# Performance work log

Hardware: AMD Instinct MI355X
Metric: run time of the kernel (lower is better)

The kernel has to match this reference:

```python
import jax, jax.numpy as jnp
import numpy as np

D = 1024        # embed_dim
NH = 16         # num_heads
DH = D // NH    # head_dim
FFN = 2048      # ffn_hidden_dim
E = 8           # num_experts
K = 2           # top_k
B, T = 2, 1024


def setup_inputs() -> dict:
    key = jax.random.key(0)
    ks = jax.random.split(key, 6)
    s = 0.02
    return {
        "x": jax.random.normal(ks[0], (B, T, D), jnp.float32),
        "ln1_g": jnp.ones((D,), jnp.float32),
        "ln1_b": jnp.zeros((D,), jnp.float32),
        "qkv_w": jax.random.normal(ks[1], (D, 3 * D), jnp.float32) * s,   # [in,out]
        "out_w": jax.random.normal(ks[2], (D, D), jnp.float32) * s,
        "ln2_g": jnp.ones((D,), jnp.float32),
        "ln2_b": jnp.zeros((D,), jnp.float32),
        "gate_w": jax.random.normal(ks[3], (D, E), jnp.float32) * s,
        "expert_biases": jnp.zeros((E,), jnp.float32),
        "w1": jax.random.normal(ks[4], (E, D, 2 * FFN), jnp.float32) * s,  # Expert.linear1 stacked
        "w2": jax.random.normal(ks[5], (E, FFN, D), jnp.float32) * s,      # Expert.linear2 stacked
    }


def _layernorm(x, g, b, eps=1e-5):
    mu = x.mean(-1, keepdims=True)
    var = ((x - mu) ** 2).mean(-1, keepdims=True)
    return (x - mu) * jax.lax.rsqrt(var + eps) * g + b


def _rope(x, theta=10000.0):
    # x: [B, T, H, Dh]; torchtune-style interleaved (even, odd) pair rotation, input_pos=None -> 0..T-1
    Tt, Dh = x.shape[1], x.shape[3]
    inv = 1.0 / (theta ** (jnp.arange(0, Dh, 2, dtype=jnp.float32) / Dh))   # [Dh/2]
    ang = jnp.arange(Tt, dtype=jnp.float32)[:, None] * inv[None, :]         # [T, Dh/2]
    cos = jnp.cos(ang)[None, :, None, :]
    sin = jnp.sin(ang)[None, :, None, :]
    x1, x2 = x[..., 0::2], x[..., 1::2]
    return jnp.stack([x1 * cos - x2 * sin, x2 * cos + x1 * sin], axis=-1).reshape(x.shape)


def reference(x, ln1_g, ln1_b, qkv_w, out_w, ln2_g, ln2_b, gate_w, expert_biases, w1, w2):
    Bx, Tx, Dx = x.shape
    # --- attention sub-block ---
    xn = _layernorm(x, ln1_g, ln1_b)
    qkv = (xn @ qkv_w).reshape(Bx, Tx, 3, NH, DH)
    q, k, v = qkv[:, :, 0], qkv[:, :, 1], qkv[:, :, 2]
    q, k = _rope(q), _rope(k)
    q = q.transpose(0, 2, 1, 3)  # [B,H,T,Dh]
    k = k.transpose(0, 2, 1, 3)
    v = v.transpose(0, 2, 1, 3)
    scores = jnp.einsum('bhqd,bhkd->bhqk', q, k) / jnp.sqrt(jnp.float32(DH))
    attn = jax.nn.softmax(scores, axis=-1)   # non-causal (SDPA default)
    o = jnp.einsum('bhqk,bhkd->bhqd', attn, v).transpose(0, 2, 1, 3).reshape(Bx, Tx, Dx)
    x = x + o @ out_w

    # --- MoE sub-block ---
    xn2 = _layernorm(x, ln2_g, ln2_b)
    gate_scores = xn2 @ gate_w + expert_biases             # [B,T,E]
    topk_vals, topk_idx = jax.lax.top_k(gate_scores, K)    # [B,T,K]
    gates = jax.nn.softmax(topk_vals, axis=-1)             # [B,T,K]
    oh = jax.nn.one_hot(topk_idx, E, dtype=x.dtype)        # [B,T,K,E]
    comb = (oh * gates[..., None]).sum(2)                  # [B,T,E] combine weights
    # dense per-expert SwiGLU FFN (equivalent to masked dispatch: unrouted weight = 0)
    h = jnp.einsum('btd,edh->beth', xn2, w1)               # [B,E,T,2*FFN]
    h1, h2 = jnp.split(h, 2, axis=-1)
    act = jax.nn.silu(h1) * h2
    eo = jnp.einsum('beth,ehd->betd', act, w2)             # [B,E,T,D]
    ffn_out = jnp.einsum('bte,betd->btd', comb, eo)
    x = x + ffn_out

    # --- load-balancing loss ---
    usage = oh.sum((0, 1, 2))                              # [E] token counts
    usage_ratio = usage / usage.sum()
    probs = jax.nn.softmax(gate_scores, axis=-1).mean((0, 1))
    prob_ratio = probs / probs.sum()
    lb_loss = (usage_ratio * prob_ratio).sum() * E
    return x, lb_loss
```

## Files before the change

kernel.cpp:

```cpp
#include <hip/hip_runtime.h>
#include <hip/hip_fp16.h>


typedef _Float16 half8 __attribute__((ext_vector_type(8)));
typedef float f32x4 __attribute__((ext_vector_type(4)));

#define DI __device__ __forceinline__

struct Desc { int e, base, rows; };

DI float blockReduceSum(float v, float* red) {
#pragma unroll
    for (int m = 32; m; m >>= 1) v += __shfl_xor(v, m);
    int w = threadIdx.x >> 6;
    if ((threadIdx.x & 63) == 0) red[w] = v;
    __syncthreads();
    v = red[0] + red[1] + red[2] + red[3];
    __syncthreads();
    return v;
}

DI void split2(float v, __half& hi, __half& lo) {
    hi = __float2half(v);
    lo = __float2half((v - __half2float(hi)) * 2048.0f);
}

enum { EPI_RESID = 0, EPI_QKV = 1 };

template<int WM, int WN, int FM, int FN, int EPI>
__global__ __launch_bounds__(256, 2)
void k_gemm_pk(const __half* __restrict__ Ah, const __half* __restrict__ Al, int lda,
               const __half* __restrict__ Bh, const __half* __restrict__ Bl, int ldb,
               float* __restrict__ Cf, int ldc, int M, int N, int K,
               const float* __restrict__ resid,
               __half* __restrict__ qh_p, __half* __restrict__ ql_p,
               __half* __restrict__ kh_p, __half* __restrict__ kl_p,
               __half* __restrict__ vth_p, __half* __restrict__ vtl_p,
               const float* __restrict__ rc, const float* __restrict__ rs)
{
    constexpr int BM = WM * FM * 16, BN = WN * FN * 16;
    constexpr int PITCH = 40;
    __shared__ __half AsH[BM * PITCH], AsL[BM * PITCH];
    __shared__ __half BsH[BN * PITCH], BsL[BN * PITCH];
    const int tid = threadIdx.x;
    const int lane = tid & 63, w = tid >> 6;
    const int l15 = lane & 15, g = lane >> 4;
    const int wm = w / WN, wn = w % WN;
    const int m0 = blockIdx.x * BM, n0 = blockIdx.y * BN;

    f32x4 acc0[FM][FN] = {}; f32x4 acc1[FM][FN] = {};

    for (int k0 = 0; k0 < K; k0 += 32) {
        __syncthreads();
#pragma unroll
        for (int it = 0; it < BM / 64; ++it) {
            int c = it * 256 + tid, row = c >> 2, kg = c & 3;
            long src = (long)(m0 + row) * lda + k0 + kg * 8;
            *(uint4*)&AsH[row * PITCH + kg * 8] = *(const uint4*)(Ah + src);
            *(uint4*)&AsL[row * PITCH + kg * 8] = *(const uint4*)(Al + src);
        }
#pragma unroll
        for (int it = 0; it < BN / 64; ++it) {
            int c = it * 256 + tid, row = c >> 2, kg = c & 3;
            long src = (long)(n0 + row) * ldb + k0 + kg * 8;
            *(uint4*)&BsH[row * PITCH + kg * 8] = *(const uint4*)(Bh + src);
            *(uint4*)&BsL[row * PITCH + kg * 8] = *(const uint4*)(Bl + src);
        }
        __syncthreads();
        half8 ah[FM], al[FM];
#pragma unroll
        for (int i = 0; i < FM; ++i) {
            int ar = (wm * FM * 16 + i * 16 + l15) * PITCH + g * 8;
            ah[i] = *(const half8*)&AsH[ar];
            al[i] = *(const half8*)&AsL[ar];
        }
#pragma unroll
        for (int n = 0; n < FN; ++n) {
            int br = (wn * FN * 16 + n * 16 + l15) * PITCH + g * 8;
            half8 bh = *(const half8*)&BsH[br];
            half8 bl = *(const half8*)&BsL[br];
#pragma unroll
            for (int i = 0; i < FM; ++i) {
                acc0[i][n] = __builtin_amdgcn_mfma_f32_16x16x32_f16(ah[i], bh, acc0[i][n], 0, 0, 0);
                acc1[i][n] = __builtin_amdgcn_mfma_f32_16x16x32_f16(ah[i], bl, acc1[i][n], 0, 0, 0);
                acc1[i][n] = __builtin_amdgcn_mfma_f32_16x16x32_f16(al[i], bh, acc1[i][n], 0, 0, 0);
            }
        }
    }

#pragma unroll
    for (int i = 0; i < FM; ++i)
#pragma unroll
    for (int n = 0; n < FN; ++n)
#pragma unroll
    for (int j = 0; j < 4; ++j) {
        float v = acc0[i][n][j] + acc1[i][n][j] * (1.0f / 2048.0f);
        int gm = m0 + wm * FM * 16 + i * 16 + g * 4 + j;
        int gn = n0 + wn * FN * 16 + n * 16 + l15;
        if constexpr (EPI == EPI_RESID) {
            Cf[(long)gm * ldc + gn] = v + resid[(long)gm * ldc + gn];
        } else {
            int t = gm & 1023, b = gm >> 10;
            float vp = __shfl_xor(v, 1);
            if (gn < 2048) {
                int col = gn & 1023;
                int i2 = (col & 63) >> 1;
                float cv = rc[t * 32 + i2], sv = rs[t * 32 + i2];
                float rot = cv * v + sv * ((lane & 1) ? vp : -vp);
                __half hi_, lo_; split2(rot, hi_, lo_);
                long o = ((long)(b * 16 + (col >> 6)) * 1024 + t) * 64 + (col & 63);
                if (gn < 1024) { qh_p[o] = hi_; ql_p[o] = lo_; }
                else           { kh_p[o] = hi_; kl_p[o] = lo_; }
            } else {
                int col = gn - 2048;
                __half hi_, lo_; split2(v, hi_, lo_);
                long o = ((long)(b * 16 + (col >> 6)) * 64 + (col & 63)) * 1024 + t;
                vth_p[o] = hi_; vtl_p[o] = lo_;
            }
        }
    }
}

__global__ __launch_bounds__(256, 2)
void k_flash(const __half* __restrict__ qh_g, const __half* __restrict__ ql_g,
             const __half* __restrict__ kh_g, const __half* __restrict__ kl_g,
             const __half* __restrict__ vth_g, const __half* __restrict__ vtl_g,
             __half* __restrict__ oh_g, __half* __restrict__ ol_g)
{
    constexpr int P = 72;
    __shared__ __half KsH[64 * P], KsL[64 * P], VsH[64 * P], VsL[64 * P], PsH[64 * P], PsL[64 * P];
    const int tid = threadIdx.x, lane = tid & 63, w = tid >> 6;
    const int l15 = lane & 15, g = lane >> 4;
    const int q0 = blockIdx.x * 64;
    const int bh = blockIdx.y;
    const long base = (long)bh * 65536;

    half8 qhi[2], qlo[2];
    {
        long qoff = base + (long)(q0 + w * 16 + l15) * 64 + g * 8;
        qhi[0] = *(const half8*)(qh_g + qoff); qhi[1] = *(const half8*)(qh_g + qoff + 32);
        qlo[0] = *(const half8*)(ql_g + qoff); qlo[1] = *(const half8*)(ql_g + qoff + 32);
    }

    float m_[4] = {-1e30f, -1e30f, -1e30f, -1e30f};
    float l_[4] = {0.f, 0.f, 0.f, 0.f};
    f32x4 o0[4] = {}, o1[4] = {};

    for (int kt = 0; kt < 16; ++kt) {
        __syncthreads();
#pragma unroll
        for (int it = 0; it < 2; ++it) {
            int c = it * 256 + tid, row = c >> 3, kg = c & 7;
            long src = base + (long)(kt * 64 + row) * 64 + kg * 8;
            *(uint4*)&KsH[row * P + kg * 8] = *(const uint4*)(kh_g + src);
            *(uint4*)&KsL[row * P + kg * 8] = *(const uint4*)(kl_g + src);
            long vs = base + (long)row * 1024 + kt * 64 + kg * 8;
            *(uint4*)&VsH[row * P + kg * 8] = *(const uint4*)(vth_g + vs);
            *(uint4*)&VsL[row * P + kg * 8] = *(const uint4*)(vtl_g + vs);
        }
        __syncthreads();

        f32x4 s0[4] = {}, s1[4] = {};
#pragma unroll
        for (int cf = 0; cf < 4; ++cf) {
            int kr = (cf * 16 + l15) * P + g * 8;
            half8 kh0 = *(const half8*)&KsH[kr], kh1 = *(const half8*)&KsH[kr + 32];
            half8 kl0 = *(const half8*)&KsL[kr], kl1 = *(const half8*)&KsL[kr + 32];
            s0[cf] = __builtin_amdgcn_mfma_f32_16x16x32_f16(qhi[0], kh0, s0[cf], 0, 0, 0);
            s1[cf] = __builtin_amdgcn_mfma_f32_16x16x32_f16(qhi[0], kl0, s1[cf], 0, 0, 0);
            s1[cf] = __builtin_amdgcn_mfma_f32_16x16x32_f16(qlo[0], kh0, s1[cf], 0, 0, 0);
            s0[cf] = __builtin_amdgcn_mfma_f32_16x16x32_f16(qhi[1], kh1, s0[cf], 0, 0, 0);
            s1[cf] = __builtin_amdgcn_mfma_f32_16x16x32_f16(qhi[1], kl1, s1[cf], 0, 0, 0);
            s1[cf] = __builtin_amdgcn_mfma_f32_16x16x32_f16(qlo[1], kh1, s1[cf], 0, 0, 0);
        }

#pragma unroll
        for (int j = 0; j < 4; ++j) {
            float sv[4];
#pragma unroll
            for (int cf = 0; cf < 4; ++cf)
                sv[cf] = (s0[cf][j] + s1[cf][j] * (1.0f / 2048.0f)) * 0.125f;
            float mx = fmaxf(fmaxf(sv[0], sv[1]), fmaxf(sv[2], sv[3]));
#pragma unroll
            for (int msk = 8; msk; msk >>= 1) mx = fmaxf(mx, __shfl_xor(mx, msk));
            float mn = fmaxf(m_[j], mx);
            float r = expf(m_[j] - mn);
            m_[j] = mn;
            float rs = 0.f;
#pragma unroll
            for (int cf = 0; cf < 4; ++cf) {
                float p = expf(sv[cf] - mn);
                rs += p;
                __half hi_, lo_; split2(p, hi_, lo_);
                PsH[(w * 16 + g * 4 + j) * P + cf * 16 + l15] = hi_;
                PsL[(w * 16 + g * 4 + j) * P + cf * 16 + l15] = lo_;
            }
#pragma unroll
            for (int msk = 8; msk; msk >>= 1) rs += __shfl_xor(rs, msk);
            l_[j] = l_[j] * r + rs;
#pragma unroll
            for (int df = 0; df < 4; ++df) { o0[df][j] *= r; o1[df][j] *= r; }
        }
        __syncthreads();

        int pr = (w * 16 + l15) * P + g * 8;
        half8 ph0 = *(const half8*)&PsH[pr], ph1 = *(const half8*)&PsH[pr + 32];
        half8 pl0 = *(const half8*)&PsL[pr], pl1 = *(const half8*)&PsL[pr + 32];
#pragma unroll
        for (int df = 0; df < 4; ++df) {
            int vr = (df * 16 + l15) * P + g * 8;
            half8 vh0 = *(const half8*)&VsH[vr], vh1 = *(const half8*)&VsH[vr + 32];
            half8 vl0 = *(const half8*)&VsL[vr], vl1 = *(const half8*)&VsL[vr + 32];
            o0[df] = __builtin_amdgcn_mfma_f32_16x16x32_f16(ph0, vh0, o0[df], 0, 0, 0);
            o1[df] = __builtin_amdgcn_mfma_f32_16x16x32_f16(ph0, vl0, o1[df], 0, 0, 0);
            o1[df] = __builtin_amdgcn_mfma_f32_16x16x32_f16(pl0, vh0, o1[df], 0, 0, 0);
            o0[df] = __builtin_amdgcn_mfma_f32_16x16x32_f16(ph1, vh1, o0[df], 0, 0, 0);
            o1[df] = __builtin_amdgcn_mfma_f32_16x16x32_f16(ph1, vl1, o1[df], 0, 0, 0);
            o1[df] = __builtin_amdgcn_mfma_f32_16x16x32_f16(pl1, vh1, o1[df], 0, 0, 0);
        }
    }

    float invl[4];
#pragma unroll
    for (int j = 0; j < 4; ++j) invl[j] = 1.0f / l_[j];
    const int b = bh >> 4, hh = bh & 15;
#pragma unroll
    for (int df = 0; df < 4; ++df)
#pragma unroll
    for (int j = 0; j < 4; ++j) {
        float v = (o0[df][j] + o1[df][j] * (1.0f / 2048.0f)) * invl[j];
        long orow = (long)b * 1024 + q0 + w * 16 + g * 4 + j;
        int col = hh * 64 + df * 16 + l15;
        __half hi_, lo_; split2(v, hi_, lo_);
        oh_g[orow * 1024 + col] = hi_;
        ol_g[orow * 1024 + col] = lo_;
    }
}

__global__ __launch_bounds__(256) void k_wconv(const float* __restrict__ src,
                                               __half* __restrict__ dst, int R, int C)
{
    src += (long)blockIdx.z * R * C;
    dst += (long)blockIdx.z * R * C;
    __shared__ float t[64][65];
    const int tid = threadIdx.x;
    const int c0 = blockIdx.x * 64, r0 = blockIdx.y * 64;
#pragma unroll
    for (int it = 0; it < 4; ++it) {
        int idx = it * 256 + tid;
        int r = idx >> 4, c4 = (idx & 15) * 4;
        float4 v = *(const float4*)(src + (long)(r0 + r) * C + c0 + c4);
        t[r][c4] = v.x; t[r][c4 + 1] = v.y; t[r][c4 + 2] = v.z; t[r][c4 + 3] = v.w;
    }
    __syncthreads();
#pragma unroll
    for (int it = 0; it < 2; ++it) {
        int idx = it * 256 + tid;
        int orow = idx >> 3, oc = (idx & 7) * 8;
        __half v[8];
#pragma unroll
        for (int j = 0; j < 8; ++j) v[j] = __float2half(t[oc + j][orow]);
        *(uint4*)(dst + (long)(c0 + orow) * R + r0 + oc) = *(uint4*)v;
    }
}

template<bool GATHER, int MODE, int FM, int FN, int WN>
__global__ __launch_bounds__(256, 4)
void k_gemm_moe(const __half* __restrict__ A, int lda, const int* __restrict__ rowidx,
                const Desc* __restrict__ desc, const int* __restrict__ ntiles,
                const __half* __restrict__ Bbase, long sB, int ldb,
                void* __restrict__ Cv, int K, const __half* __restrict__ zp)
{
    if ((int)blockIdx.x >= *ntiles) return;
    Desc d = desc[blockIdx.x];
    const __half* Bp = Bbase + (long)d.e * sB;
    constexpr int WM = 4 / WN;
    constexpr int BM = WM * FM * 16, BN = WN * FN * 16;
    constexpr int ACH = BM / 16, BCH = BN / 16;
    constexpr int NCH = ACH + BCH;
    constexpr int CPW = NCH / 4;
    constexpr int HALF_PER_BUF = NCH * 512;
    __shared__ __half S[2][HALF_PER_BUF];
    const int tid = threadIdx.x, lane = tid & 63, w = tid >> 6;
    const int l15 = lane & 15, g = lane >> 4;
    const int wm = w / WN, wn = w % WN;
    const int n0 = blockIdx.y * (MODE == 0 ? BN / 2 : BN);

    const int dlt = lane >> 2;
    const int kgs = ((lane & 3) ^ ((lane >> 3) & 3)) * 8;
    const __half* src[CPW];
    int loff[CPW];
#pragma unroll
    for (int ci = 0; ci < CPW; ++ci) {
        int chunk = w * CPW + ci;
        loff[ci] = chunk * 512;
        if (chunk < ACH) {
            int row = chunk * 16 + dlt;
            if constexpr (GATHER) {
                bool valid = row < d.rows;
                int ar = valid ? rowidx[d.base + row] : 0;
                src[ci] = valid ? (A + (long)ar * lda + kgs) : (zp + kgs);
            } else {
                src[ci] = A + (long)(d.base + row) * lda + kgs;
            }
        } else {
            int row = (chunk - ACH) * 16 + dlt;
            int srcrow;
            if constexpr (MODE == 0) {
                int pb = row >> 4, w4 = row & 15;
                srcrow = ((pb & 1) ? 2048 : 0) + n0 + (pb >> 1) * 16 + w4;
            } else {
                srcrow = n0 + row;
            }
            src[ci] = Bp + (long)srcrow * ldb + kgs;
        }
    }

    const int sg = (g ^ ((l15 >> 1) & 3)) * 8;
    const int arow = (wm * FM * 16 + l15) * 32 + sg;
    const int brow = BM * 32 + (wn * FN * 16 + l15) * 32 + sg;

#pragma unroll
    for (int ci = 0; ci < CPW; ++ci)
        __builtin_amdgcn_global_load_lds((const void*)(src[ci]),
                                         (void*)&S[0][loff[ci]], 16, 0, 0);
    __syncthreads();

    f32x4 acc[FM][FN] = {};
    int cur = 0;
    for (int k0 = 0; k0 < K; k0 += 32) {
        if (k0 + 32 < K) {
            const __half* sb = &S[cur ^ 1][0];
#pragma unroll
            for (int ci = 0; ci < CPW; ++ci)
                __builtin_amdgcn_global_load_lds((const void*)(src[ci] + k0 + 32),
                                                 (void*)(sb + loff[ci]), 16, 0, 0);
        }
        const __half* sc = &S[cur][0];
        half8 a[FM];
#pragma unroll
        for (int i = 0; i < FM; ++i)
            a[i] = *(const half8*)(sc + arow + i * 512);
#pragma unroll
        for (int n = 0; n < FN; ++n) {
            half8 b = *(const half8*)(sc + brow + n * 512);
#pragma unroll
            for (int i = 0; i < FM; ++i)
                acc[i][n] = __builtin_amdgcn_mfma_f32_16x16x32_f16(a[i], b, acc[i][n], 0, 0, 0);
        }
        __syncthreads();
        cur ^= 1;
    }

    if constexpr (MODE == 0) {
#pragma unroll
        for (int i = 0; i < FM; ++i)
#pragma unroll
        for (int p = 0; p < FN / 2; ++p)
#pragma unroll
        for (int j = 0; j < 4; ++j) {
            int rl = wm * FM * 16 + i * 16 + g * 4 + j;
            float h1 = acc[i][2 * p][j], h2 = acc[i][2 * p + 1][j];
            float a = h1 / (1.0f + expf(-h1)) * h2;
            if (rl >= d.rows) a = 0.0f;
            int jc = n0 + wn * (FN * 8) + p * 16 + l15;
            ((__half*)Cv)[(long)(d.base + rl) * 2048 + jc] = __float2half(a);
        }
    } else {
#pragma unroll
        for (int i = 0; i < FM; ++i)
#pragma unroll
        for (int n = 0; n < FN; ++n)
#pragma unroll
        for (int j = 0; j < 4; ++j) {
            int rl = wm * FM * 16 + i * 16 + g * 4 + j;
            int gn = n0 + wn * FN * 16 + n * 16 + l15;
            ((float*)Cv)[(long)(d.base + rl) * 1024 + gn] = acc[i][n][j];
        }
    }
}

__global__ __launch_bounds__(256) void k_transpose_pk(const float* __restrict__ src,
    __half* __restrict__ dsth, __half* __restrict__ dstl, int R, int C)
{
    __shared__ float t[64][65];
    const int tid = threadIdx.x;
    const int c0 = blockIdx.x * 64, r0 = blockIdx.y * 64;
#pragma unroll
    for (int it = 0; it < 4; ++it) {
        int idx = it * 256 + tid;
        int r = idx >> 4, c4 = (idx & 15) * 4;
        float4 v = *(const float4*)(src + (long)(r0 + r) * C + c0 + c4);
        t[r][c4] = v.x; t[r][c4 + 1] = v.y; t[r][c4 + 2] = v.z; t[r][c4 + 3] = v.w;
    }
    __syncthreads();
#pragma unroll
    for (int it = 0; it < 4; ++it) {
        int idx = it * 256 + tid;
        int orow = idx >> 4, oc = (idx & 15) * 4;
        __half hs[4], ls[4];
#pragma unroll
        for (int m = 0; m < 4; ++m) split2(t[oc + m][orow], hs[m], ls[m]);
        long o = (long)(c0 + orow) * R + r0 + oc;
        *(uint2*)&dsth[o] = *(uint2*)hs;
        *(uint2*)&dstl[o] = *(uint2*)ls;
    }
}

template<int MODE>
__global__ __launch_bounds__(256) void k_ln(const float* __restrict__ X,
    const float* __restrict__ g, const float* __restrict__ bta,
    void* __restrict__ o1, void* __restrict__ o2)
{
    __shared__ float red[4];
    const long row = blockIdx.x;
    const float* xr = X + row * 1024;
    const int c = threadIdx.x * 4;
    float4 v = *(const float4*)(xr + c);
    float mu = blockReduceSum(v.x + v.y + v.z + v.w, red) * (1.0f / 1024.0f);
    float d0 = v.x - mu, d1 = v.y - mu, d2 = v.z - mu, d3 = v.w - mu;
    float var = blockReduceSum(d0 * d0 + d1 * d1 + d2 * d2 + d3 * d3, red) * (1.0f / 1024.0f);
    float rs = 1.0f / sqrtf(var + 1e-5f);
    float4 gv = *(const float4*)(g + c);
    float4 bv = *(const float4*)(bta + c);
    float y[4] = {d0 * rs * gv.x + bv.x, d1 * rs * gv.y + bv.y,
                  d2 * rs * gv.z + bv.z, d3 * rs * gv.w + bv.w};
    if constexpr (MODE == 0) {
        __half hs[4], ls[4];
#pragma unroll
        for (int m = 0; m < 4; ++m) split2(y[m], hs[m], ls[m]);
        *(uint2*)((__half*)o1 + row * 1024 + c) = *(uint2*)hs;
        *(uint2*)((__half*)o2 + row * 1024 + c) = *(uint2*)ls;
    } else {
        *(float4*)((float*)o1 + row * 1024 + c) = make_float4(y[0], y[1], y[2], y[3]);
        __half hs[4];
#pragma unroll
        for (int m = 0; m < 4; ++m) hs[m] = __float2half(y[m]);
        *(uint2*)((__half*)o2 + row * 1024 + c) = *(uint2*)hs;
    }
}

__global__ __launch_bounds__(256) void k_rope_table(float* __restrict__ ct, float* __restrict__ st)
{
    int idx = blockIdx.x * 256 + threadIdx.x;
    int t = idx >> 5, i = idx & 31;
    float inv = 1.0f / (float)pow(10000.0, (double)i / 32.0);
    float ang = (float)t * inv;
    ct[idx] = cosf(ang);
    st[idx] = sinf(ang);
}

__global__ __launch_bounds__(256) void k_gate(const float* __restrict__ xn2,
    const float* __restrict__ gw, const float* __restrict__ eb,
    int* __restrict__ topidx, float* __restrict__ gates,
    float* __restrict__ pprob)
{
    __shared__ float pp[4][8];
    const int lane = threadIdx.x & 63, w = threadIdx.x >> 6;
    const int t = blockIdx.x * 4 + w;
    const float* xr = xn2 + (long)t * 1024;
    float sc[8] = {0, 0, 0, 0, 0, 0, 0, 0};
#pragma unroll
    for (int i = 0; i < 4; ++i) {
        int d = i * 256 + lane * 4;
        float4 xv = *(const float4*)(xr + d);
        float xa[4] = {xv.x, xv.y, xv.z, xv.w};
#pragma unroll
        for (int j = 0; j < 4; ++j) {
            float xx = xa[j];
            const float4* gp = (const float4*)(gw + (long)(d + j) * 8);
            float4 g0 = gp[0], g1 = gp[1];
            sc[0] += xx * g0.x; sc[1] += xx * g0.y; sc[2] += xx * g0.z; sc[3] += xx * g0.w;
            sc[4] += xx * g1.x; sc[5] += xx * g1.y; sc[6] += xx * g1.z; sc[7] += xx * g1.w;
        }
    }
#pragma unroll
    for (int e = 0; e < 8; ++e) {
#pragma unroll
        for (int m = 32; m; m >>= 1) sc[e] += __shfl_xor(sc[e], m);
        sc[e] += eb[e];
    }
    if (lane == 0) {
        int i1 = 0; float v1 = sc[0];
        for (int e = 1; e < 8; ++e) if (sc[e] > v1) { v1 = sc[e]; i1 = e; }
        int i2 = (i1 == 0) ? 1 : 0; float v2 = sc[i2];
        for (int e = 0; e < 8; ++e) if (e != i1 && sc[e] > v2) { v2 = sc[e]; i2 = e; }
        float e2 = expf(v2 - v1);
        gates[t * 2] = 1.0f / (1.0f + e2);
        gates[t * 2 + 1] = e2 / (1.0f + e2);
        topidx[t * 2] = i1; topidx[t * 2 + 1] = i2;
        float mxx = sc[0];
        for (int e = 1; e < 8; ++e) mxx = fmaxf(mxx, sc[e]);
        float se = 0.0f, pe[8];
        for (int e = 0; e < 8; ++e) { pe[e] = expf(sc[e] - mxx); se += pe[e]; }
        float inv = 1.0f / se;
        for (int e = 0; e < 8; ++e) pp[w][e] = pe[e] * inv;
    }
    __syncthreads();
    if (threadIdx.x < 8)
        pprob[(long)blockIdx.x * 8 + threadIdx.x] =
            pp[0][threadIdx.x] + pp[1][threadIdx.x] + pp[2][threadIdx.x] + pp[3][threadIdx.x];
}

__global__ __launch_bounds__(256) void k_route(const int* __restrict__ topidx,
    int* __restrict__ rowidx, int* __restrict__ invpos,
    int* __restrict__ ntiles, Desc* __restrict__ desc, int* __restrict__ cnt)
{
    __shared__ int cnt_s[8], base_s[8], fill[8];
    const int tid = threadIdx.x;
    if (tid < 8) { cnt_s[tid] = 0; fill[tid] = 0; }
    __syncthreads();
    for (int i = tid; i < 4096; i += 256)
        atomicAdd(&cnt_s[topidx[i]], 1);
    __syncthreads();
    if (tid == 0) {
        int tl[8]; int running = 0, maxT = 0;
        for (int e = 0; e < 8; ++e) {
            int ce = cnt_s[e];
            cnt[e] = ce;
            base_s[e] = running;
            tl[e] = (ce + 127) >> 7;
            running += tl[e] * 128;
            if (tl[e] > maxT) maxT = tl[e];
        }
        int nt = 0;
        for (int r = 0; r < maxT; ++r)
            for (int e = 0; e < 8; ++e)
                if (r < tl[e]) {
                    desc[nt].e = e;
                    desc[nt].base = base_s[e] + r * 128;
                    desc[nt].rows = min(128, cnt_s[e] - r * 128);
                    ++nt;
                }
        *ntiles = nt;
    }
    __syncthreads();
    for (int t = tid; t < 2048; t += 256) {
#pragma unroll
        for (int s = 0; s < 2; ++s) {
            int e = topidx[t * 2 + s];
            int p = base_s[e] + atomicAdd(&fill[e], 1);
            rowidx[p] = t;
            invpos[t * 2 + s] = p;
        }
    }
}

__global__ __launch_bounds__(256) void k_combine(const float* __restrict__ x1,
    const float* __restrict__ eo, const int* __restrict__ invpos,
    const float* __restrict__ gates, float* __restrict__ out)
{
    const int t = blockIdx.x, c = threadIdx.x * 4;
    float g0 = gates[t * 2], g1 = gates[t * 2 + 1];
    int p0 = invpos[t * 2], p1 = invpos[t * 2 + 1];
    float4 xv = *(const float4*)(x1 + (long)t * 1024 + c);
    float4 e0 = *(const float4*)(eo + (long)p0 * 1024 + c);
    float4 e1 = *(const float4*)(eo + (long)p1 * 1024 + c);
    float4 o;
    o.x = xv.x + g0 * e0.x + g1 * e1.x;
    o.y = xv.y + g0 * e0.y + g1 * e1.y;
    o.z = xv.z + g0 * e0.z + g1 * e1.z;
    o.w = xv.w + g0 * e0.w + g1 * e1.w;
    *(float4*)(out + (long)t * 1024 + c) = o;
}

__global__ __launch_bounds__(256) void k_loss(const int* __restrict__ cnt,
    const float* __restrict__ pprob, float* __restrict__ out)
{
    __shared__ float m[32][8];
    const int tid = threadIdx.x;
    const int e = tid & 7, g = tid >> 3;
    float local = 0.0f;
    for (int b = g; b < 512; b += 32) local += pprob[b * 8 + e];
    m[g][e] = local;
    __syncthreads();
    if (tid == 0) {
        float us = 0, ps = 0, pe[8], ue[8];
        for (int ee = 0; ee < 8; ++ee) {
            float s = 0;
            for (int gg = 0; gg < 32; ++gg) s += m[gg][ee];
            pe[ee] = s; ps += s;
            ue[ee] = (float)cnt[ee]; us += ue[ee];
        }
        float lb = 0;
        for (int ee = 0; ee < 8; ++ee) lb += (ue[ee] / us) * (pe[ee] / ps);
        out[2097152] = lb * 8.0f;
    }
}

extern "C" void kernel_launch(void* const* d_in, const int* in_sizes, int n_in,
                              void* d_out, int out_size, void* d_ws, size_t ws_size,
                              hipStream_t stream)
{
    const float* x    = (const float*)d_in[0];
    const float* ln1g = (const float*)d_in[1];
    const float* ln1b = (const float*)d_in[2];
    const float* qkvw = (const float*)d_in[3];
    const float* outw = (const float*)d_in[4];
    const float* ln2g = (const float*)d_in[5];
    const float* ln2b = (const float*)d_in[6];
    const float* gw   = (const float*)d_in[7];
    const float* eb   = (const float*)d_in[8];
    const float* w1   = (const float*)d_in[9];
    const float* w2   = (const float*)d_in[10];
    float* out = (float*)d_out;
    char* ws = (char*)d_ws;

    constexpr size_t OFF_QWTH = 0;
    constexpr size_t OFF_QWTL = 6291456;
    constexpr size_t OFF_OWTH = 12582912;
    constexpr size_t OFF_OWTL = 14680064;
    constexpr size_t OFF_XN1H = 16777216;
    constexpr size_t OFF_XN1L = 20971520;
    constexpr size_t OFF_QH   = 25165824;
    constexpr size_t OFF_QL   = 29360128;
    constexpr size_t OFF_KH   = 33554432;
    constexpr size_t OFF_KL   = 37748736;
    constexpr size_t OFF_VTH  = 41943040;
    constexpr size_t OFF_VTL  = 46137344;
    constexpr size_t OFF_OH   = 50331648;
    constexpr size_t OFF_OL   = 54525952;
    constexpr size_t OFF_X1   = 58720256;
    constexpr size_t OFF_XN2F = 67108864;
    constexpr size_t OFF_XN2H = 75497472;
    constexpr size_t OFF_RC   = 79691776;
    constexpr size_t OFF_RS   = 79822848;
    constexpr size_t OFF_IDX  = 79953920;
    constexpr size_t OFF_GATES= 79970304;
    constexpr size_t OFF_INVP = 79986688;
    constexpr size_t OFF_ROWI = 80003072;
    constexpr size_t OFF_CNT  = 80023552;
    constexpr size_t OFF_NT   = 80023616;
    constexpr size_t OFF_DESC = 80023680;
    constexpr size_t OFF_PPROB= 80024704;
    constexpr size_t OFF_ACT  = 80041984;
    constexpr size_t OFF_EO   = 101013504;
    constexpr size_t OFF_W1T  = 121985024;
    constexpr size_t OFF_W2T  = 189093888;

    __half* qwth = (__half*)(ws + OFF_QWTH);
    __half* qwtl = (__half*)(ws + OFF_QWTL);
    __half* owth = (__half*)(ws + OFF_OWTH);
    __half* owtl = (__half*)(ws + OFF_OWTL);
    __half* xn1h = (__half*)(ws + OFF_XN1H);
    __half* xn1l = (__half*)(ws + OFF_XN1L);
    __half* qh   = (__half*)(ws + OFF_QH);
    __half* ql   = (__half*)(ws + OFF_QL);
    __half* kh   = (__half*)(ws + OFF_KH);
    __half* kl   = (__half*)(ws + OFF_KL);
    __half* vth  = (__half*)(ws + OFF_VTH);
    __half* vtl  = (__half*)(ws + OFF_VTL);
    __half* oh   = (__half*)(ws + OFF_OH);
    __half* ol   = (__half*)(ws + OFF_OL);
    float* x1    = (float*)(ws + OFF_X1);
    float* xn2f  = (float*)(ws + OFF_XN2F);
    __half* xn2h = (__half*)(ws + OFF_XN2H);
    float* rc    = (float*)(ws + OFF_RC);
    float* rs    = (float*)(ws + OFF_RS);
    int*   idx   = (int*)(ws + OFF_IDX);
    float* gates = (float*)(ws + OFF_GATES);
    int*   invp  = (int*)(ws + OFF_INVP);
    int*   rowi  = (int*)(ws + OFF_ROWI);
    int*   cnt   = (int*)(ws + OFF_CNT);
    int*   nt    = (int*)(ws + OFF_NT);
    Desc*  desc  = (Desc*)(ws + OFF_DESC);
    float* pprob = (float*)(ws + OFF_PPROB);
    __half* act  = (__half*)(ws + OFF_ACT);
    float* eo    = (float*)(ws + OFF_EO);
    __half* w1t  = (__half*)(ws + OFF_W1T);
    __half* w2t  = (__half*)(ws + OFF_W2T);
    __half* zp   = xn1h;

    k_transpose_pk<<<dim3(48, 16, 1), 256, 0, stream>>>(qkvw, qwth, qwtl, 1024, 3072);
    k_transpose_pk<<<dim3(16, 16, 1), 256, 0, stream>>>(outw, owth, owtl, 1024, 1024);
    k_wconv<<<dim3(64, 16, 8), 256, 0, stream>>>(w1, w1t, 1024, 4096);
    k_wconv<<<dim3(16, 32, 8), 256, 0, stream>>>(w2, w2t, 2048, 1024);
    k_rope_table<<<dim3(128), 256, 0, stream>>>(rc, rs);

    k_ln<0><<<dim3(2048), 256, 0, stream>>>(x, ln1g, ln1b, xn1h, xn1l);

    k_gemm_pk<2, 2, 2, 4, EPI_QKV><<<dim3(32, 24, 1), 256, 0, stream>>>(
        xn1h, xn1l, 1024, qwth, qwtl, 1024, nullptr, 0, 2048, 3072, 1024,
        nullptr, qh, ql, kh, kl, vth, vtl, rc, rs);

    hipMemsetAsync(zp, 0, 4096, stream);

    k_flash<<<dim3(16, 32, 1), 256, 0, stream>>>(qh, ql, kh, kl, vth, vtl, oh, ol);

    k_gemm_pk<2, 2, 2, 2, EPI_RESID><<<dim3(32, 16, 1), 256, 0, stream>>>(
        oh, ol, 1024, owth, owtl, 1024, x1, 1024, 2048, 1024, 1024,
        x, nullptr, nullptr, nullptr, nullptr, nullptr, nullptr, nullptr, nullptr);

    k_ln<1><<<dim3(2048), 256, 0, stream>>>(x1, ln2g, ln2b, xn2f, xn2h);

    k_gate<<<dim3(512), 256, 0, stream>>>(xn2f, gw, eb, idx, gates, pprob);
    k_route<<<dim3(1), 256, 0, stream>>>(idx, rowi, invp, nt, desc, cnt);

    k_gemm_moe<true, 0, 4, 4, 2><<<dim3(40, 32, 1), 256, 0, stream>>>(
        xn2h, 1024, rowi, desc, nt, w1t, 4194304, 1024, act, 1024, zp);

    k_gemm_moe<false, 1, 2, 4, 1><<<dim3(40, 16, 1), 256, 0, stream>>>(
        act, 2048, nullptr, desc, nt, w2t, 2097152, 2048, eo, 2048, zp);

    k_combine<<<dim3(2048), 256, 0, stream>>>(x1, eo, invp, gates, out);
    k_loss<<<dim3(1), 256, 0, stream>>>(cnt, pprob, out);
}
```

Baseline: 380.8 us.

## Swizzle flash-attention LDS, raise occupancy, and use explicit vmcnt waits in GEMM

The flash kernel drops its padded LDS rows (stride 72) in favour of an XOR-swizzled 64-wide layout for K, V and P. This shrinks LDS use, and launch bounds are raised to allow three blocks per CU. The GEMM main loop swaps the full __syncthreads for explicit s_waitcnt vmcnt counts plus raw s_barrier, so the next tile's global_load_lds stays in flight while the current tile is consumed. This risks correctness if the vmcnt counts don't match the number of outstanding loads, and the tighter register budget could cause spills.

```diff
diff --git a/kernel.cpp b/kernel.cpp
--- a/kernel.cpp
+++ b/kernel.cpp
@@ -8,6 +8,14 @@
 #define DI __device__ __forceinline__
 
 struct Desc { int e, base, rows; };
+
+template<int N> DI void waitcnt_vm() {
+    if constexpr (N == 0)      asm volatile("s_waitcnt vmcnt(0)" ::: "memory");
+    else if constexpr (N == 3) asm volatile("s_waitcnt vmcnt(3)" ::: "memory");
+    else if constexpr (N == 4) asm volatile("s_waitcnt vmcnt(4)" ::: "memory");
+    else if constexpr (N == 6) asm volatile("s_waitcnt vmcnt(6)" ::: "memory");
+    else if constexpr (N == 8) asm volatile("s_waitcnt vmcnt(8)" ::: "memory");
+}
 
 DI float blockReduceSum(float v, float* red) {
 #pragma unroll
@@ -121,14 +129,14 @@
     }
 }
 
-__global__ __launch_bounds__(256, 2)
+__global__ __launch_bounds__(256, 3)
 void k_flash(const __half* __restrict__ qh_g, const __half* __restrict__ ql_g,
              const __half* __restrict__ kh_g, const __half* __restrict__ kl_g,
              const __half* __restrict__ vth_g, const __half* __restrict__ vtl_g,
              __half* __restrict__ oh_g, __half* __restrict__ ol_g)
 {
-    constexpr int P = 72;
-    __shared__ __half KsH[64 * P], KsL[64 * P], VsH[64 * P], VsL[64 * P], PsH[64 * P], PsL[64 * P];
+    __shared__ __half KsH[64 * 64], KsL[64 * 64], VsH[64 * 64], VsL[64 * 64],
+                      PsH[64 * 64], PsL[64 * 64];
     const int tid = threadIdx.x, lane = tid & 63, w = tid >> 6;
     const int l15 = lane & 15, g = lane >> 4;
     const int q0 = blockIdx.x * 64;
@@ -151,21 +159,23 @@
 #pragma unroll
         for (int it = 0; it < 2; ++it) {
             int c = it * 256 + tid, row = c >> 3, kg = c & 7;
+            int sw = (kg ^ (row & 7)) * 8;
             long src = base + (long)(kt * 64 + row) * 64 + kg * 8;
-            *(uint4*)&KsH[row * P + kg * 8] = *(const uint4*)(kh_g + src);
-            *(uint4*)&KsL[row * P + kg * 8] = *(const uint4*)(kl_g + src);
+            *(uint4*)&KsH[row * 64 + sw] = *(const uint4*)(kh_g + src);
+            *(uint4*)&KsL[row * 64 + sw] = *(const uint4*)(kl_g + src);
             long vs = base + (long)row * 1024 + kt * 64 + kg * 8;
-            *(uint4*)&VsH[row * P + kg * 8] = *(const uint4*)(vth_g + vs);
-            *(uint4*)&VsL[row * P + kg * 8] = *(const uint4*)(vtl_g + vs);
+            *(uint4*)&VsH[row * 64 + sw] = *(const uint4*)(vth_g + vs);
+            *(uint4*)&VsL[row * 64 + sw] = *(const uint4*)(vtl_g + vs);
         }
         __syncthreads();
 
         f32x4 s0[4] = {}, s1[4] = {};
 #pragma unroll
         for (int cf = 0; cf < 4; ++cf) {
-            int kr = (cf * 16 + l15) * P + g * 8;
-            half8 kh0 = *(const half8*)&KsH[kr], kh1 = *(const half8*)&KsH[kr + 32];
-            half8 kl0 = *(const half8*)&KsL[kr], kl1 = *(const half8*)&KsL[kr + 32];
+            int rr = cf * 16 + l15, rb = rr * 64, rx = rr & 7;
+            int s0o = rb + ((g ^ rx) * 8), s1o = rb + (((g + 4) ^ rx) * 8);
+            half8 kh0 = *(const half8*)&KsH[s0o], kh1 = *(const half8*)&KsH[s1o];
+            half8 kl0 = *(const half8*)&KsL[s0o], kl1 = *(const half8*)&KsL[s1o];
             s0[cf] = __builtin_amdgcn_mfma_f32_16x16x32_f16(qhi[0], kh0, s0[cf], 0, 0, 0);
             s1[cf] = __builtin_amdgcn_mfma_f32_16x16x32_f16(qhi[0], kl0, s1[cf], 0, 0, 0);
             s1[cf] = __builtin_amdgcn_mfma_f32_16x16x32_f16(qlo[0], kh0, s1[cf], 0, 0, 0);
@@ -187,13 +197,16 @@
             float r = expf(m_[j] - mn);
             m_[j] = mn;
             float rs = 0.f;
+            int prow = w * 16 + g * 4 + j, pb = prow * 64, px = prow & 7;
 #pragma unroll
             for (int cf = 0; cf < 4; ++cf) {
                 float p = expf(sv[cf] - mn);
                 rs += p;
                 __half hi_, lo_; split2(p, hi_, lo_);
-                PsH[(w * 16 + g * 4 + j) * P + cf * 16 + l15] = hi_;
-                PsL[(w * 16 + g * 4 + j) * P + cf * 16 + l15] = lo_;
+                int pgl = cf * 16 + l15;
+                int po = pb + ((pgl >> 3) ^ px) * 8 + (pgl & 7);
+                PsH[po] = hi_;
+                PsL[po] = lo_;
             }
 #pragma unroll
             for (int msk = 8; msk; msk >>= 1) rs += __shfl_xor(rs, msk);
@@ -203,14 +216,16 @@
         }
         __syncthreads();
 
-        int pr = (w * 16 + l15) * P + g * 8;
-        half8 ph0 = *(const half8*)&PsH[pr], ph1 = *(const half8*)&PsH[pr + 32];
-        half8 pl0 = *(const half8*)&PsL[pr], pl1 = *(const half8*)&PsL[pr + 32];
+        int rrp = w * 16 + l15, pbr = rrp * 64, pxr = rrp & 7;
+        int p0o = pbr + ((g ^ pxr) * 8), p1o = pbr + (((g + 4) ^ pxr) * 8);
+        half8 ph0 = *(const half8*)&PsH[p0o], ph1 = *(const half8*)&PsH[p1o];
+        half8 pl0 = *(const half8*)&PsL[p0o], pl1 = *(const half8*)&PsL[p1o];
 #pragma unroll
         for (int df = 0; df < 4; ++df) {
-            int vr = (df * 16 + l15) * P + g * 8;
-            half8 vh0 = *(const half8*)&VsH[vr], vh1 = *(const half8*)&VsH[vr + 32];
-            half8 vl0 = *(const half8*)&VsL[vr], vl1 = *(const half8*)&VsL[vr + 32];
+            int rr = df * 16 + l15, rb = rr * 64, rx = rr & 7;
+            int v0o = rb + ((g ^ rx) * 8), v1o = rb + (((g + 4) ^ rx) * 8);
+            half8 vh0 = *(const half8*)&VsH[v0o], vh1 = *(const half8*)&VsH[v1o];
+            half8 vl0 = *(const half8*)&VsL[v0o], vl1 = *(const half8*)&VsL[v1o];
             o0[df] = __builtin_amdgcn_mfma_f32_16x16x32_f16(ph0, vh0, o0[df], 0, 0, 0);
             o1[df] = __builtin_amdgcn_mfma_f32_16x16x32_f16(ph0, vl0, o1[df], 0, 0, 0);
             o1[df] = __builtin_amdgcn_mfma_f32_16x16x32_f16(pl0, vh0, o1[df], 0, 0, 0);
@@ -324,7 +339,6 @@
     for (int ci = 0; ci < CPW; ++ci)
         __builtin_amdgcn_global_load_lds((const void*)(src[ci]),
                                          (void*)&S[0][loff[ci]], 16, 0, 0);
-    __syncthreads();
 
     f32x4 acc[FM][FN] = {};
     int cur = 0;
@@ -335,7 +349,13 @@
             for (int ci = 0; ci < CPW; ++ci)
                 __builtin_amdgcn_global_load_lds((const void*)(src[ci] + k0 + 32),
                                                  (void*)(sb + loff[ci]), 16, 0, 0);
-        }
+            waitcnt_vm<CPW>();
+        } else {
+            waitcnt_vm<0>();
+        }
+        __builtin_amdgcn_s_barrier();
+        __builtin_amdgcn_sched_barrier(0);
+
         const __half* sc = &S[cur][0];
         half8 a[FM];
 #pragma unroll
@@ -348,7 +368,7 @@
             for (int i = 0; i < FM; ++i)
                 acc[i][n] = __builtin_amdgcn_mfma_f32_16x16x32_f16(a[i], b, acc[i][n], 0, 0, 0);
         }
-        __syncthreads();
+        __builtin_amdgcn_s_barrier();
         cur ^= 1;
     }
 
```

Result: slower. 394.4 us (+3.6%).
